# Performance work log

Measured on AMD Instinct MI355X. Metric: run time of the kernel, lower is better.

Reference implementation:

```python
import jax, jax.numpy as jnp
import numpy as np

B, M, D = 256, 256, 16
H1, H2 = 64, 64
HN = H1 // 2  # split_half keeps first half as next-layer state


def setup_inputs() -> dict:
    key = jax.random.key(0)
    ks = jax.random.split(key, 8)
    x = jax.random.normal(ks[0], (B, M), dtype=jnp.float32)
    emb = 0.02 * jax.random.normal(ks[1], (M, D), dtype=jnp.float32)  # field_embedding
    # Conv1d(kernel=1) weights squeezed to [out_ch, in_ch]
    def xavier(k, o, i):
        lim = np.sqrt(6.0 / (o + i)).astype(np.float32)
        return jax.random.uniform(k, (o, i), dtype=jnp.float32, minval=-lim, maxval=lim)
    W0 = xavier(ks[2], H1, M * M)      # layer 0: in_ch = m*m
    b0 = jnp.zeros((H1,), dtype=jnp.float32)
    W1 = xavier(ks[3], H2, HN * M)     # layer 1: in_ch = (H1//2)*m
    b1 = jnp.zeros((H2,), dtype=jnp.float32)
    out_width = (H1 - HN) + H2         # 32 + 64 = 96
    fcW = xavier(ks[4], 2, out_width)
    fcb = jnp.zeros((2,), dtype=jnp.float32)
    return {"x": x, "emb": emb, "W0": W0, "b0": b0, "W1": W1, "b1": b1, "fcW": fcW, "fcb": fcb}


def _cin_layer(Xk_prev, X0, W, b):
    # outer product over fields, flattened: Z [B, prev_H*m, d]
    Bd = X0.shape[0]
    Z = jnp.einsum('bhd,bmd->bhmd', Xk_prev, X0).reshape(Bd, -1, X0.shape[-1])
    # kernel-1 Conv1d == channel-mixing matmul per d slice, + bias, + relu
    return jax.nn.relu(jnp.einsum('bcd,oc->bod', Z, W) + b[None, :, None])


def reference(x, emb, W0, b0, W1, b1, fcW, fcb):
    X0 = jnp.einsum('bi,ij->bij', x, emb)          # [B, m, d]
    X1 = _cin_layer(X0, X0, W0, b0)                # [B, H1, d]
    out1 = X1[:, HN:, :]                            # direct output half
    Xp = X1[:, :HN, :]                              # hidden half feeds next layer
    X2 = _cin_layer(Xp, X0, W1, b1)                # [B, H2, d] (last layer: full output)
    cin_out = jnp.concatenate([out1.sum(axis=2), X2.sum(axis=2)], axis=1)  # [B, 96]
    return cin_out @ fcW.T + fcb
```

## Files before the change

### kernel.cpp

```cpp
#include <hip/hip_runtime.h>

typedef unsigned short u16;
typedef short bf16x8 __attribute__((ext_vector_type(8)));
typedef float f32x4 __attribute__((ext_vector_type(4)));

#define AS1 __attribute__((address_space(1)))
#define AS3 __attribute__((address_space(3)))

__device__ __forceinline__ u16 f2bf(float f) {
    unsigned u = __float_as_uint(f);
    u += 0x7fffu + ((u >> 16) & 1u);
    return (u16)(u >> 16);
}
__device__ __forceinline__ float bf2f(u16 h) {
    return __uint_as_float(((unsigned)h) << 16);
}

__device__ __forceinline__ void gload_lds16(const void* g, void* l) {
    __builtin_amdgcn_global_load_lds((AS1 unsigned int*)(g),
                                     (AS3 unsigned int*)(l), 16, 0, 0);
}

__global__ void cvt_bf16_kernel(const float* __restrict__ W0, const float* __restrict__ W1,
                                u16* __restrict__ W0b, u16* __restrict__ W1b) {
    int i = blockIdx.x * blockDim.x + threadIdx.x;
    const float* src; u16* dst; int j;
    if (i < 1048576) { src = W0; dst = W0b; j = i; }
    else             { src = W1; dst = W1b; j = i - 1048576; }
    float4 v = reinterpret_cast<const float4*>(src)[j];
    ushort4 o;
    o.x = f2bf(v.x); o.y = f2bf(v.y); o.z = f2bf(v.z); o.w = f2bf(v.w);
    reinterpret_cast<ushort4*>(dst)[j] = o;
}

__global__ void build_qt_kernel(const float* __restrict__ x, const float* __restrict__ emb,
                                u16* __restrict__ Qt, u16* __restrict__ E1) {
    int n = blockIdx.x;
    int b = n >> 4, d = n & 15;
    int m0 = threadIdx.x * 4;
    float4 xv = *reinterpret_cast<const float4*>(x + b * 256 + m0);
    ushort4 q;
    q.x = f2bf(xv.x * emb[(m0 + 0) * 16 + d]);
    q.y = f2bf(xv.y * emb[(m0 + 1) * 16 + d]);
    q.z = f2bf(xv.z * emb[(m0 + 2) * 16 + d]);
    q.w = f2bf(xv.w * emb[(m0 + 3) * 16 + d]);
    *reinterpret_cast<ushort4*>(Qt + n * 256 + m0) = q;
    int e1 = (n >> 8) * 65536 + (m0 >> 7) * 32768 + ((n >> 6) & 3) * 8192
           + ((m0 >> 4) & 7) * 1024 + ((n >> 4) & 3) * 256
           + ((((m0 >> 2) & 3) << 4) + (n & 15)) * 4;
    *reinterpret_cast<ushort4*>(E1 + e1) = q;
}

__global__ __launch_bounds__(512, 2) void cin1_kernel(
    const u16* __restrict__ W0b, const u16* __restrict__ Qt, const u16* __restrict__ E1,
    const float* __restrict__ b0, u16* __restrict__ E2, float* __restrict__ S1)
{
    __shared__ __attribute__((aligned(16))) u16 As[4][8192];
    __shared__ __attribute__((aligned(16))) u16 Bs[4][8192];
    __shared__ float part[2][256];

    const int tid = threadIdx.x, lane = tid & 63, w = tid >> 6;
    const int wh = w >> 2, wn = w & 3;
    const int lid = blockIdx.x;
    const int g8 = lid & 7, m = lid >> 3;
    const int o = ((g8 >> 1) << 4) | (m & 15);
    const int ntile = ((g8 & 1) << 3) | (m >> 4);

    const int dr = ((lane >> 3) << 1) | (lane & 1);
    const int dk = (((lane & 7) >> 1) ^ ((lane >> 3) & 3)) << 3;
    const u16* aSrc0 = W0b + (o * 256 + (w * 2 + 0) * 16 + dr) * 256 + dk;
    const u16* aSrc1 = W0b + (o * 256 + (w * 2 + 1) * 16 + dr) * 256 + dk;
    const u16* bSrc0 = Qt + (ntile * 256 + (w * 2 + 0) * 16 + dr) * 256 + dk;
    const u16* bSrc1 = Qt + (ntile * 256 + (w * 2 + 1) * 16 + dr) * 256 + dk;
    const int ldsA0 = (w * 2 + 0) * 512, ldsA1 = (w * 2 + 1) * 512;

    const int l2 = (lane & 15) >> 1;
    const int qu = (((((lane >> 4) ^ (l2 & 3)) << 1) | (lane & 1)) << 3);
    const int aOff = wh * 4096 + l2 * 64 + qu;
    const int bOff = wn * 2048 + l2 * 64 + qu;

    f32x4 zero = {0.f, 0.f, 0.f, 0.f};
    f32x4 acc[8][4];
#pragma unroll
    for (int f = 0; f < 8; ++f)
#pragma unroll
        for (int gg = 0; gg < 4; ++gg) acc[f][gg] = zero;

    auto stage = [&](int kc, int bb) {
        int ko = kc * 32;
        gload_lds16(aSrc0 + ko, &As[bb][ldsA0]);
        gload_lds16(aSrc1 + ko, &As[bb][ldsA1]);
        gload_lds16(bSrc0 + ko, &Bs[bb][ldsA0]);
        gload_lds16(bSrc1 + ko, &Bs[bb][ldsA1]);
    };

    stage(0, 0); stage(1, 1); stage(2, 2);
#pragma unroll
    for (int kc = 0; kc < 8; ++kc) {
        if (kc < 6)       asm volatile("s_waitcnt vmcnt(8)" ::: "memory");
        else if (kc == 6) asm volatile("s_waitcnt vmcnt(4)" ::: "memory");
        else              asm volatile("s_waitcnt vmcnt(0)" ::: "memory");
        __builtin_amdgcn_s_barrier();
        asm volatile("" ::: "memory");
        const u16* Ab = &As[kc & 3][0];
        const u16* Bb = &Bs[kc & 3][0];
        bf16x8 a[8], b[4];
#pragma unroll
        for (int f = 0; f < 8; ++f)
            a[f] = *reinterpret_cast<const bf16x8*>(Ab + aOff + f * 512);
#pragma unroll
        for (int gg = 0; gg < 4; ++gg)
            b[gg] = *reinterpret_cast<const bf16x8*>(Bb + bOff + gg * 512);
#pragma unroll
        for (int f = 0; f < 8; ++f)
#pragma unroll
            for (int gg = 0; gg < 4; ++gg)
                acc[f][gg] = __builtin_amdgcn_mfma_f32_16x16x32_bf16(a[f], b[gg], acc[f][gg], 0, 0, 0);
        if (kc < 5) stage(kc + 3, (kc + 3) & 3);
    }

    float psum[4] = {0.f, 0.f, 0.f, 0.f};
    const u16* eb = E1 + ntile * 65536 + wh * 32768 + wn * 8192 + lane * 4;
#pragma unroll
    for (int f = 0; f < 8; ++f)
#pragma unroll
        for (int gg = 0; gg < 4; ++gg) {
            ushort4 wv = *reinterpret_cast<const ushort4*>(eb + f * 1024 + gg * 256);
            psum[gg] += bf2f(wv.x) * acc[f][gg][0] + bf2f(wv.y) * acc[f][gg][1]
                      + bf2f(wv.z) * acc[f][gg][2] + bf2f(wv.w) * acc[f][gg][3];
        }
#pragma unroll
    for (int gg = 0; gg < 4; ++gg) {
        float p = psum[gg];
        p += __shfl_xor(p, 16);
        p += __shfl_xor(p, 32);
        if (lane < 16) part[wh][wn * 64 + gg * 16 + lane] = p;
    }
    __syncthreads();
    if (tid < 256) {
        const int nl = tid;
        float v = part[0][nl] + part[1][nl] + b0[o];
        float r = fmaxf(v, 0.0f);
        const int n = ntile * 256 + nl;
        if (o < 32) {
            int idx = ntile * 8192 + (o >> 4) * 4096 + (nl >> 6) * 1024 + ((nl >> 4) & 3) * 256
                    + ((((o >> 2) & 3) << 4) + (nl & 15)) * 4 + (o & 3);
            E2[idx] = f2bf(r);
        } else {
            float s = r;
            s += __shfl_xor(s, 1); s += __shfl_xor(s, 2);
            s += __shfl_xor(s, 4); s += __shfl_xor(s, 8);
            if ((nl & 15) == 0) S1[(n >> 4) * 32 + (o - 32)] = s;
        }
    }
}

__global__ __launch_bounds__(512, 2) void cin2_kernel(
    const u16* __restrict__ W1b, const u16* __restrict__ Qt, const u16* __restrict__ E2,
    const float* __restrict__ b1, float* __restrict__ S2)
{
    __shared__ __attribute__((aligned(16))) u16 As[4][4096];
    __shared__ __attribute__((aligned(16))) u16 Bs[4][8192];
    __shared__ float part[2][2][256];

    const int tid = threadIdx.x, lane = tid & 63, w = tid >> 6;
    const int wh = w >> 2, wn = w & 3;
    const int ntile = blockIdx.x & 15, og = blockIdx.x >> 4;

    const int dr = ((lane >> 3) << 1) | (lane & 1);
    const int dk = (((lane & 7) >> 1) ^ ((lane >> 3) & 3)) << 3;
    const u16* aSrc = W1b + (og * 128 + w * 16 + dr) * 256 + dk;
    const u16* bSrc0 = Qt + (ntile * 256 + (w * 2 + 0) * 16 + dr) * 256 + dk;
    const u16* bSrc1 = Qt + (ntile * 256 + (w * 2 + 1) * 16 + dr) * 256 + dk;
    const int ldsA = w * 512;
    const int ldsB0 = (w * 2 + 0) * 512, ldsB1 = (w * 2 + 1) * 512;

    const int l2 = (lane & 15) >> 1;
    const int qu = (((((lane >> 4) ^ (l2 & 3)) << 1) | (lane & 1)) << 3);
    const int aOff = wh * 2048 + l2 * 64 + qu;
    const int bOff = wn * 2048 + l2 * 64 + qu;

    f32x4 zero = {0.f, 0.f, 0.f, 0.f};
    f32x4 acc[4][4];
#pragma unroll
    for (int f = 0; f < 4; ++f)
#pragma unroll
        for (int gg = 0; gg < 4; ++gg) acc[f][gg] = zero;

    auto stage = [&](int kc, int bb) {
        int ko = kc * 32;
        gload_lds16(aSrc + ko, &As[bb][ldsA]);
        gload_lds16(bSrc0 + ko, &Bs[bb][ldsB0]);
        gload_lds16(bSrc1 + ko, &Bs[bb][ldsB1]);
    };

    stage(0, 0); stage(1, 1); stage(2, 2);
#pragma unroll
    for (int kc = 0; kc < 8; ++kc) {
        if (kc < 6)       asm volatile("s_waitcnt vmcnt(6)" ::: "memory");
        else if (kc == 6) asm volatile("s_waitcnt vmcnt(3)" ::: "memory");
        else              asm volatile("s_waitcnt vmcnt(0)" ::: "memory");
        __builtin_amdgcn_s_barrier();
        asm volatile("" ::: "memory");
        const u16* Ab = &As[kc & 3][0];
        const u16* Bb = &Bs[kc & 3][0];
        bf16x8 a[4], b[4];
#pragma unroll
        for (int f = 0; f < 4; ++f)
            a[f] = *reinterpret_cast<const bf16x8*>(Ab + aOff + f * 512);
#pragma unroll
        for (int gg = 0; gg < 4; ++gg)
            b[gg] = *reinterpret_cast<const bf16x8*>(Bb + bOff + gg * 512);
#pragma unroll
        for (int f = 0; f < 4; ++f)
#pragma unroll
            for (int gg = 0; gg < 4; ++gg)
                acc[f][gg] = __builtin_amdgcn_mfma_f32_16x16x32_bf16(a[f], b[gg], acc[f][gg], 0, 0, 0);
        if (kc < 5) stage(kc + 3, (kc + 3) & 3);
    }

    float psum[2][4] = {{0.f,0.f,0.f,0.f},{0.f,0.f,0.f,0.f}};
    const u16* eb = E2 + ntile * 8192 + wn * 1024 + lane * 4;
#pragma unroll
    for (int f = 0; f < 4; ++f)
#pragma unroll
        for (int gg = 0; gg < 4; ++gg) {
            ushort4 wv = *reinterpret_cast<const ushort4*>(eb + (f & 1) * 4096 + gg * 256);
            psum[f >> 1][gg] += bf2f(wv.x) * acc[f][gg][0] + bf2f(wv.y) * acc[f][gg][1]
                              + bf2f(wv.z) * acc[f][gg][2] + bf2f(wv.w) * acc[f][gg][3];
        }
#pragma unroll
    for (int ol = 0; ol < 2; ++ol)
#pragma unroll
        for (int gg = 0; gg < 4; ++gg) {
            float p = psum[ol][gg];
            p += __shfl_xor(p, 16);
            p += __shfl_xor(p, 32);
            if (lane < 16) part[wh][ol][wn * 64 + gg * 16 + lane] = p;
        }
    __syncthreads();
    if (tid < 256) {
        const int nl = tid;
        const int n = ntile * 256 + nl;
#pragma unroll
        for (int ol4 = 0; ol4 < 4; ++ol4) {
            const int oo = og * 4 + ol4;
            float v = part[ol4 >> 1][ol4 & 1][nl] + b1[oo];
            float r = fmaxf(v, 0.0f);
            float s = r;
            s += __shfl_xor(s, 1); s += __shfl_xor(s, 2);
            s += __shfl_xor(s, 4); s += __shfl_xor(s, 8);
            if ((nl & 15) == 0) S2[(n >> 4) * 64 + oo] = s;
        }
    }
}

__global__ void final_fc_kernel(const float* __restrict__ S1, const float* __restrict__ S2,
                                const float* __restrict__ fcW, const float* __restrict__ fcb,
                                float* __restrict__ out) {
    int b = threadIdx.x;
    float a0 = fcb[0], a1 = fcb[1];
#pragma unroll 8
    for (int c = 0; c < 32; ++c) {
        float v = S1[b * 32 + c];
        a0 += v * fcW[c]; a1 += v * fcW[96 + c];
    }
#pragma unroll 8
    for (int c = 0; c < 64; ++c) {
        float v = S2[b * 64 + c];
        a0 += v * fcW[32 + c]; a1 += v * fcW[96 + 32 + c];
    }
    out[b * 2 + 0] = a0;
    out[b * 2 + 1] = a1;
}

extern "C" void kernel_launch(void* const* d_in, const int* in_sizes, int n_in,
                              void* d_out, int out_size, void* d_ws, size_t ws_size,
                              hipStream_t stream) {
    const float* x   = (const float*)d_in[0];
    const float* emb = (const float*)d_in[1];
    const float* W0  = (const float*)d_in[2];
    const float* b0  = (const float*)d_in[3];
    const float* W1  = (const float*)d_in[4];
    const float* b1  = (const float*)d_in[5];
    const float* fcW = (const float*)d_in[6];
    const float* fcb = (const float*)d_in[7];
    float* out = (float*)d_out;

    char* ws = (char*)d_ws;
    u16*   W0b = (u16*)(ws);
    u16*   W1b = (u16*)(ws + 8388608);
    u16*   Qt  = (u16*)(ws + 9437184);
    u16*   E1  = (u16*)(ws + 11534336);
    u16*   E2  = (u16*)(ws + 13631488);
    float* S1  = (float*)(ws + 13893632);
    float* S2  = (float*)(ws + 13926400);

    cvt_bf16_kernel<<<4608, 256, 0, stream>>>(W0, W1, W0b, W1b);
    build_qt_kernel<<<4096, 64, 0, stream>>>(x, emb, Qt, E1);
    cin1_kernel<<<1024, 512, 0, stream>>>(W0b, Qt, E1, b0, E2, S1);
    cin2_kernel<<<256, 512, 0, stream>>>(W1b, Qt, E2, b1, S2);
    final_fc_kernel<<<1, 256, 0, stream>>>(S1, S2, fcW, fcb, out);
}
```

Baseline: 70.81 us.

## Merge prep kernels and double-buffer LDS fragment reads in CIN GEMMs

Measured after the change: 72.34 us. 1.02x slower.

```diff
diff --git a/kernel.cpp b/kernel.cpp
--- a/kernel.cpp
+++ b/kernel.cpp
@@ -21,34 +21,37 @@
                                      (AS3 unsigned int*)(l), 16, 0, 0);
 }
 
-__global__ void cvt_bf16_kernel(const float* __restrict__ W0, const float* __restrict__ W1,
-                                u16* __restrict__ W0b, u16* __restrict__ W1b) {
-    int i = blockIdx.x * blockDim.x + threadIdx.x;
-    const float* src; u16* dst; int j;
-    if (i < 1048576) { src = W0; dst = W0b; j = i; }
-    else             { src = W1; dst = W1b; j = i - 1048576; }
-    float4 v = reinterpret_cast<const float4*>(src)[j];
-    ushort4 o;
-    o.x = f2bf(v.x); o.y = f2bf(v.y); o.z = f2bf(v.z); o.w = f2bf(v.w);
-    reinterpret_cast<ushort4*>(dst)[j] = o;
-}
-
-__global__ void build_qt_kernel(const float* __restrict__ x, const float* __restrict__ emb,
-                                u16* __restrict__ Qt, u16* __restrict__ E1) {
-    int n = blockIdx.x;
-    int b = n >> 4, d = n & 15;
-    int m0 = threadIdx.x * 4;
-    float4 xv = *reinterpret_cast<const float4*>(x + b * 256 + m0);
-    ushort4 q;
-    q.x = f2bf(xv.x * emb[(m0 + 0) * 16 + d]);
-    q.y = f2bf(xv.y * emb[(m0 + 1) * 16 + d]);
-    q.z = f2bf(xv.z * emb[(m0 + 2) * 16 + d]);
-    q.w = f2bf(xv.w * emb[(m0 + 3) * 16 + d]);
-    *reinterpret_cast<ushort4*>(Qt + n * 256 + m0) = q;
-    int e1 = (n >> 8) * 65536 + (m0 >> 7) * 32768 + ((n >> 6) & 3) * 8192
-           + ((m0 >> 4) & 7) * 1024 + ((n >> 4) & 3) * 256
-           + ((((m0 >> 2) & 3) << 4) + (n & 15)) * 4;
-    *reinterpret_cast<ushort4*>(E1 + e1) = q;
+__global__ void prep_kernel(const float* __restrict__ W0, const float* __restrict__ W1,
+                            const float* __restrict__ x, const float* __restrict__ emb,
+                            u16* __restrict__ W0b, u16* __restrict__ W1b,
+                            u16* __restrict__ Qt, u16* __restrict__ E1) {
+    int gid = blockIdx.x;
+    if (gid < 4608) {
+        int i = gid * 256 + threadIdx.x;
+        const float* src; u16* dst; int j;
+        if (i < 1048576) { src = W0; dst = W0b; j = i; }
+        else             { src = W1; dst = W1b; j = i - 1048576; }
+        float4 v = reinterpret_cast<const float4*>(src)[j];
+        ushort4 o;
+        o.x = f2bf(v.x); o.y = f2bf(v.y); o.z = f2bf(v.z); o.w = f2bf(v.w);
+        reinterpret_cast<ushort4*>(dst)[j] = o;
+    } else {
+        int n = (gid - 4608) * 4 + (threadIdx.x >> 6);
+        int lane = threadIdx.x & 63;
+        int b = n >> 4, d = n & 15;
+        int m0 = lane * 4;
+        float4 xv = *reinterpret_cast<const float4*>(x + b * 256 + m0);
+        ushort4 q;
+        q.x = f2bf(xv.x * emb[(m0 + 0) * 16 + d]);
+        q.y = f2bf(xv.y * emb[(m0 + 1) * 16 + d]);
+        q.z = f2bf(xv.z * emb[(m0 + 2) * 16 + d]);
+        q.w = f2bf(xv.w * emb[(m0 + 3) * 16 + d]);
+        *reinterpret_cast<ushort4*>(Qt + n * 256 + m0) = q;
+        int e1 = (n >> 8) * 65536 + (m0 >> 7) * 32768 + ((n >> 6) & 3) * 8192
+               + ((m0 >> 4) & 7) * 1024 + ((n >> 4) & 3) * 256
+               + ((((m0 >> 2) & 3) << 4) + (n & 15)) * 4;
+        *reinterpret_cast<ushort4*>(E1 + e1) = q;
+    }
 }
 
 __global__ __launch_bounds__(512, 2) void cin1_kernel(
@@ -86,6 +89,8 @@
 #pragma unroll
         for (int gg = 0; gg < 4; ++gg) acc[f][gg] = zero;
 
+    bf16x8 a[2][8], b[2][4];
+
     auto stage = [&](int kc, int bb) {
         int ko = kc * 32;
         gload_lds16(aSrc0 + ko, &As[bb][ldsA0]);
@@ -94,30 +99,41 @@
         gload_lds16(bSrc1 + ko, &Bs[bb][ldsA1]);
     };
 
+#define PREREAD(kb, pb)                                                              \
+    {                                                                                \
+        const u16* Ab_ = &As[(kb) & 3][0];                                           \
+        const u16* Bb_ = &Bs[(kb) & 3][0];                                           \
+        _Pragma("unroll")                                                            \
+        for (int f_ = 0; f_ < 8; ++f_)                                               \
+            a[pb][f_] = *reinterpret_cast<const bf16x8*>(Ab_ + aOff + f_ * 512);     \
+        _Pragma("unroll")                                                            \
+        for (int g_ = 0; g_ < 4; ++g_)                                               \
+            b[pb][g_] = *reinterpret_cast<const bf16x8*>(Bb_ + bOff + g_ * 512);     \
+    }
+
     stage(0, 0); stage(1, 1); stage(2, 2);
+    asm volatile("s_waitcnt vmcnt(8)" ::: "memory");
+    __builtin_amdgcn_s_barrier();
+    asm volatile("" ::: "memory");
+    PREREAD(0, 0);
 #pragma unroll
     for (int kc = 0; kc < 8; ++kc) {
-        if (kc < 6)       asm volatile("s_waitcnt vmcnt(8)" ::: "memory");
-        else if (kc == 6) asm volatile("s_waitcnt vmcnt(4)" ::: "memory");
-        else              asm volatile("s_waitcnt vmcnt(0)" ::: "memory");
+        if (kc < 6) asm volatile("s_waitcnt vmcnt(4)" ::: "memory");
+        else        asm volatile("s_waitcnt vmcnt(0)" ::: "memory");
         __builtin_amdgcn_s_barrier();
         asm volatile("" ::: "memory");
-        const u16* Ab = &As[kc & 3][0];
-        const u16* Bb = &Bs[kc & 3][0];
-        bf16x8 a[8], b[4];
+        const int cur = kc & 1;
+        if (kc < 7) PREREAD(kc + 1, cur ^ 1);
+        __builtin_amdgcn_s_setprio(1);
 #pragma unroll
         for (int f = 0; f < 8; ++f)
-            a[f] = *reinterpret_cast<const bf16x8*>(Ab + aOff + f * 512);
-#pragma unroll
-        for (int gg = 0; gg < 4; ++gg)
-            b[gg] = *reinterpret_cast<const bf16x8*>(Bb + bOff + gg * 512);
-#pragma unroll
-        for (int f = 0; f < 8; ++f)
 #pragma unroll
             for (int gg = 0; gg < 4; ++gg)
-                acc[f][gg] = __builtin_amdgcn_mfma_f32_16x16x32_bf16(a[f], b[gg], acc[f][gg], 0, 0, 0);
+                acc[f][gg] = __builtin_amdgcn_mfma_f32_16x16x32_bf16(a[cur][f], b[cur][gg], acc[f][gg], 0, 0, 0);
+        __builtin_amdgcn_s_setprio(0);
         if (kc < 5) stage(kc + 3, (kc + 3) & 3);
     }
+#undef PREREAD
 
     float psum[4] = {0.f, 0.f, 0.f, 0.f};
     const u16* eb = E1 + ntile * 65536 + wh * 32768 + wn * 8192 + lane * 4;
@@ -187,6 +203,8 @@
 #pragma unroll
         for (int gg = 0; gg < 4; ++gg) acc[f][gg] = zero;
 
+    bf16x8 a[2][4], b[2][4];
+
     auto stage = [&](int kc, int bb) {
         int ko = kc * 32;
         gload_lds16(aSrc + ko, &As[bb][ldsA]);
@@ -194,30 +212,41 @@
         gload_lds16(bSrc1 + ko, &Bs[bb][ldsB1]);
     };
 
+#define PREREAD2(kb, pb)                                                             \
+    {                                                                                \
+        const u16* Ab_ = &As[(kb) & 3][0];                                           \
+        const u16* Bb_ = &Bs[(kb) & 3][0];                                           \
+        _Pragma("unroll")                                                            \
+        for (int f_ = 0; f_ < 4; ++f_)                                               \
+            a[pb][f_] = *reinterpret_cast<const bf16x8*>(Ab_ + aOff + f_ * 512);     \
+        _Pragma("unroll")                                                            \
+        for (int g_ = 0; g_ < 4; ++g_)                                               \
+            b[pb][g_] = *reinterpret_cast<const bf16x8*>(Bb_ + bOff + g_ * 512);     \
+    }
+
     stage(0, 0); stage(1, 1); stage(2, 2);
+    asm volatile("s_waitcnt vmcnt(6)" ::: "memory");
+    __builtin_amdgcn_s_barrier();
+    asm volatile("" ::: "memory");
+    PREREAD2(0, 0);
 #pragma unroll
     for (int kc = 0; kc < 8; ++kc) {
-        if (kc < 6)       asm volatile("s_waitcnt vmcnt(6)" ::: "memory");
-        else if (kc == 6) asm volatile("s_waitcnt vmcnt(3)" ::: "memory");
-        else              asm volatile("s_waitcnt vmcnt(0)" ::: "memory");
+        if (kc < 6) asm volatile("s_waitcnt vmcnt(3)" ::: "memory");
+        else        asm volatile("s_waitcnt vmcnt(0)" ::: "memory");
         __builtin_amdgcn_s_barrier();
         asm volatile("" ::: "memory");
-        const u16* Ab = &As[kc & 3][0];
-        const u16* Bb = &Bs[kc & 3][0];
-        bf16x8 a[4], b[4];
+        const int cur = kc & 1;
+        if (kc < 7) PREREAD2(kc + 1, cur ^ 1);
+        __builtin_amdgcn_s_setprio(1);
 #pragma unroll
         for (int f = 0; f < 4; ++f)
-            a[f] = *reinterpret_cast<const bf16x8*>(Ab + aOff + f * 512);
-#pragma unroll
-        for (int gg = 0; gg < 4; ++gg)
-            b[gg] = *reinterpret_cast<const bf16x8*>(Bb + bOff + gg * 512);
-#pragma unroll
-        for (int f = 0; f < 4; ++f)
 #pragma unroll
             for (int gg = 0; gg < 4; ++gg)
-                acc[f][gg] = __builtin_amdgcn_mfma_f32_16x16x32_bf16(a[f], b[gg], acc[f][gg], 0, 0, 0);
+                acc[f][gg] = __builtin_amdgcn_mfma_f32_16x16x32_bf16(a[cur][f], b[cur][gg], acc[f][gg], 0, 0, 0);
+        __builtin_amdgcn_s_setprio(0);
         if (kc < 5) stage(kc + 3, (kc + 3) & 3);
     }
+#undef PREREAD2
 
     float psum[2][4] = {{0.f,0.f,0.f,0.f},{0.f,0.f,0.f,0.f}};
     const u16* eb = E2 + ntile * 8192 + wn * 1024 + lane * 4;
@@ -296,8 +325,7 @@
     float* S1  = (float*)(ws + 13893632);
     float* S2  = (float*)(ws + 13926400);
 
-    cvt_bf16_kernel<<<4608, 256, 0, stream>>>(W0, W1, W0b, W1b);
-    build_qt_kernel<<<4096, 64, 0, stream>>>(x, emb, Qt, E1);
+    prep_kernel<<<5632, 256, 0, stream>>>(W0, W1, x, emb, W0b, W1b, Qt, E1);
     cin1_kernel<<<1024, 512, 0, stream>>>(W0b, Qt, E1, b0, E2, S1);
     cin2_kernel<<<256, 512, 0, stream>>>(W1b, Qt, E2, b1, S2);
     final_fc_kernel<<<1, 256, 0, stream>>>(S1, S2, fcW, fcb, out);
```

## Merge prep kernels and retile CIN GEMMs to smaller N tiles with triple buffering

Applied to the files above, without the earlier changes.

Measured after the change: 71.64 us. Within noise of the previous version (+1.2%).

```diff
diff --git a/kernel.cpp b/kernel.cpp
--- a/kernel.cpp
+++ b/kernel.cpp
@@ -21,108 +21,112 @@
                                      (AS3 unsigned int*)(l), 16, 0, 0);
 }
 
-__global__ void cvt_bf16_kernel(const float* __restrict__ W0, const float* __restrict__ W1,
-                                u16* __restrict__ W0b, u16* __restrict__ W1b) {
-    int i = blockIdx.x * blockDim.x + threadIdx.x;
-    const float* src; u16* dst; int j;
-    if (i < 1048576) { src = W0; dst = W0b; j = i; }
-    else             { src = W1; dst = W1b; j = i - 1048576; }
-    float4 v = reinterpret_cast<const float4*>(src)[j];
-    ushort4 o;
-    o.x = f2bf(v.x); o.y = f2bf(v.y); o.z = f2bf(v.z); o.w = f2bf(v.w);
-    reinterpret_cast<ushort4*>(dst)[j] = o;
-}
-
-__global__ void build_qt_kernel(const float* __restrict__ x, const float* __restrict__ emb,
-                                u16* __restrict__ Qt, u16* __restrict__ E1) {
-    int n = blockIdx.x;
-    int b = n >> 4, d = n & 15;
-    int m0 = threadIdx.x * 4;
-    float4 xv = *reinterpret_cast<const float4*>(x + b * 256 + m0);
-    ushort4 q;
-    q.x = f2bf(xv.x * emb[(m0 + 0) * 16 + d]);
-    q.y = f2bf(xv.y * emb[(m0 + 1) * 16 + d]);
-    q.z = f2bf(xv.z * emb[(m0 + 2) * 16 + d]);
-    q.w = f2bf(xv.w * emb[(m0 + 3) * 16 + d]);
-    *reinterpret_cast<ushort4*>(Qt + n * 256 + m0) = q;
-    int e1 = (n >> 8) * 65536 + (m0 >> 7) * 32768 + ((n >> 6) & 3) * 8192
-           + ((m0 >> 4) & 7) * 1024 + ((n >> 4) & 3) * 256
-           + ((((m0 >> 2) & 3) << 4) + (n & 15)) * 4;
-    *reinterpret_cast<ushort4*>(E1 + e1) = q;
-}
-
-__global__ __launch_bounds__(512, 2) void cin1_kernel(
+__global__ void prep_kernel(const float* __restrict__ W0, const float* __restrict__ W1,
+                            const float* __restrict__ x, const float* __restrict__ emb,
+                            u16* __restrict__ W0b, u16* __restrict__ W1b,
+                            u16* __restrict__ Qt, u16* __restrict__ E1) {
+    int gid = blockIdx.x;
+    if (gid < 4608) {
+        int i = gid * 256 + threadIdx.x;
+        const float* src; u16* dst; int j;
+        if (i < 1048576) { src = W0; dst = W0b; j = i; }
+        else             { src = W1; dst = W1b; j = i - 1048576; }
+        float4 v = reinterpret_cast<const float4*>(src)[j];
+        ushort4 o;
+        o.x = f2bf(v.x); o.y = f2bf(v.y); o.z = f2bf(v.z); o.w = f2bf(v.w);
+        reinterpret_cast<ushort4*>(dst)[j] = o;
+    } else {
+        int n = (gid - 4608) * 4 + (threadIdx.x >> 6);
+        int lane = threadIdx.x & 63;
+        int b = n >> 4, d = n & 15;
+        int m0 = lane * 4;
+        float4 xv = *reinterpret_cast<const float4*>(x + b * 256 + m0);
+        ushort4 q;
+        q.x = f2bf(xv.x * emb[(m0 + 0) * 16 + d]);
+        q.y = f2bf(xv.y * emb[(m0 + 1) * 16 + d]);
+        q.z = f2bf(xv.z * emb[(m0 + 2) * 16 + d]);
+        q.w = f2bf(xv.w * emb[(m0 + 3) * 16 + d]);
+        *reinterpret_cast<ushort4*>(Qt + n * 256 + m0) = q;
+        int e1 = (n >> 7) * 32768 + (m0 >> 6) * 8192 + ((n >> 6) & 1) * 4096
+               + ((m0 >> 4) & 3) * 1024 + ((n >> 4) & 3) * 256
+               + (((m0 >> 2) & 3) * 16 + (n & 15)) * 4;
+        *reinterpret_cast<ushort4*>(E1 + e1) = q;
+    }
+}
+
+__global__ __launch_bounds__(512, 4) void cin1_kernel(
     const u16* __restrict__ W0b, const u16* __restrict__ Qt, const u16* __restrict__ E1,
     const float* __restrict__ b0, u16* __restrict__ E2, float* __restrict__ S1)
 {
-    __shared__ __attribute__((aligned(16))) u16 As[4][8192];
-    __shared__ __attribute__((aligned(16))) u16 Bs[4][8192];
-    __shared__ float part[2][256];
+    __shared__ __attribute__((aligned(16))) u16 As[3][8192];
+    __shared__ __attribute__((aligned(16))) u16 Bs[3][4096];
+    __shared__ float part[4][128];
 
     const int tid = threadIdx.x, lane = tid & 63, w = tid >> 6;
-    const int wh = w >> 2, wn = w & 3;
-    const int lid = blockIdx.x;
-    const int g8 = lid & 7, m = lid >> 3;
-    const int o = ((g8 >> 1) << 4) | (m & 15);
-    const int ntile = ((g8 & 1) << 3) | (m >> 4);
-
-    const int dr = ((lane >> 3) << 1) | (lane & 1);
-    const int dk = (((lane & 7) >> 1) ^ ((lane >> 3) & 3)) << 3;
-    const u16* aSrc0 = W0b + (o * 256 + (w * 2 + 0) * 16 + dr) * 256 + dk;
-    const u16* aSrc1 = W0b + (o * 256 + (w * 2 + 1) * 16 + dr) * 256 + dk;
-    const u16* bSrc0 = Qt + (ntile * 256 + (w * 2 + 0) * 16 + dr) * 256 + dk;
-    const u16* bSrc1 = Qt + (ntile * 256 + (w * 2 + 1) * 16 + dr) * 256 + dk;
+    const int wh = w >> 1, wn = w & 1;
+    const int bid = blockIdx.x;
+    const int g8 = bid & 7, rest = bid >> 3;
+    const int o = g8 * 8 + (rest & 7);
+    const int ntile = rest >> 3;
+
+    const int rl = lane >> 2;
+    const int sw = ((lane & 3) ^ ((rl + (rl >> 2)) & 3)) << 3;
+    const u16* aS0 = W0b + (o * 256 + (w * 2 + 0) * 16 + rl) * 256 + sw;
+    const u16* aS1 = W0b + (o * 256 + (w * 2 + 1) * 16 + rl) * 256 + sw;
+    const u16* bS0 = Qt + (ntile * 128 + w * 16 + rl) * 256 + sw;
     const int ldsA0 = (w * 2 + 0) * 512, ldsA1 = (w * 2 + 1) * 512;
-
-    const int l2 = (lane & 15) >> 1;
-    const int qu = (((((lane >> 4) ^ (l2 & 3)) << 1) | (lane & 1)) << 3);
-    const int aOff = wh * 4096 + l2 * 64 + qu;
-    const int bOff = wn * 2048 + l2 * 64 + qu;
+    const int ldsB0 = w * 512;
+
+    const int rbA = wh * 64 + (lane & 15);
+    const int rbB = wn * 64 + (lane & 15);
+    const int sl = lane >> 4;
+    const int aOff = rbA * 32 + ((sl ^ ((rbA + (rbA >> 2)) & 3)) << 3);
+    const int bOff = rbB * 32 + ((sl ^ ((rbB + (rbB >> 2)) & 3)) << 3);
 
     f32x4 zero = {0.f, 0.f, 0.f, 0.f};
-    f32x4 acc[8][4];
-#pragma unroll
-    for (int f = 0; f < 8; ++f)
+    f32x4 acc[4][4];
+#pragma unroll
+    for (int f = 0; f < 4; ++f)
 #pragma unroll
         for (int gg = 0; gg < 4; ++gg) acc[f][gg] = zero;
 
     auto stage = [&](int kc, int bb) {
         int ko = kc * 32;
-        gload_lds16(aSrc0 + ko, &As[bb][ldsA0]);
-        gload_lds16(aSrc1 + ko, &As[bb][ldsA1]);
-        gload_lds16(bSrc0 + ko, &Bs[bb][ldsA0]);
-        gload_lds16(bSrc1 + ko, &Bs[bb][ldsA1]);
+        gload_lds16(aS0 + ko, &As[bb][ldsA0]);
+        gload_lds16(aS1 + ko, &As[bb][ldsA1]);
+        gload_lds16(bS0 + ko, &Bs[bb][ldsB0]);
     };
 
-    stage(0, 0); stage(1, 1); stage(2, 2);
+    stage(0, 0); stage(1, 1);
 #pragma unroll
     for (int kc = 0; kc < 8; ++kc) {
-        if (kc < 6)       asm volatile("s_waitcnt vmcnt(8)" ::: "memory");
-        else if (kc == 6) asm volatile("s_waitcnt vmcnt(4)" ::: "memory");
-        else              asm volatile("s_waitcnt vmcnt(0)" ::: "memory");
+        if (kc < 7) asm volatile("s_waitcnt vmcnt(3)" ::: "memory");
+        else        asm volatile("s_waitcnt vmcnt(0)" ::: "memory");
         __builtin_amdgcn_s_barrier();
         asm volatile("" ::: "memory");
-        const u16* Ab = &As[kc & 3][0];
-        const u16* Bb = &Bs[kc & 3][0];
-        bf16x8 a[8], b[4];
-#pragma unroll
-        for (int f = 0; f < 8; ++f)
+        if (kc < 6) stage(kc + 2, (kc + 2) % 3);
+        const u16* Ab = &As[kc % 3][0];
+        const u16* Bb = &Bs[kc % 3][0];
+        bf16x8 a[4], b[4];
+#pragma unroll
+        for (int f = 0; f < 4; ++f)
             a[f] = *reinterpret_cast<const bf16x8*>(Ab + aOff + f * 512);
 #pragma unroll
         for (int gg = 0; gg < 4; ++gg)
             b[gg] = *reinterpret_cast<const bf16x8*>(Bb + bOff + gg * 512);
-#pragma unroll
-        for (int f = 0; f < 8; ++f)
+        __builtin_amdgcn_s_setprio(1);
+#pragma unroll
+        for (int f = 0; f < 4; ++f)
 #pragma unroll
             for (int gg = 0; gg < 4; ++gg)
                 acc[f][gg] = __builtin_amdgcn_mfma_f32_16x16x32_bf16(a[f], b[gg], acc[f][gg], 0, 0, 0);
-        if (kc < 5) stage(kc + 3, (kc + 3) & 3);
+        __builtin_amdgcn_s_setprio(0);
     }
 
     float psum[4] = {0.f, 0.f, 0.f, 0.f};
-    const u16* eb = E1 + ntile * 65536 + wh * 32768 + wn * 8192 + lane * 4;
-#pragma unroll
-    for (int f = 0; f < 8; ++f)
+    const u16* eb = E1 + ntile * 32768 + wh * 8192 + wn * 4096 + lane * 4;
+#pragma unroll
+    for (int f = 0; f < 4; ++f)
 #pragma unroll
         for (int gg = 0; gg < 4; ++gg) {
             ushort4 wv = *reinterpret_cast<const ushort4*>(eb + f * 1024 + gg * 256);
@@ -137,15 +141,13 @@
         if (lane < 16) part[wh][wn * 64 + gg * 16 + lane] = p;
     }
     __syncthreads();
-    if (tid < 256) {
+    if (tid < 128) {
         const int nl = tid;
-        float v = part[0][nl] + part[1][nl] + b0[o];
+        float v = part[0][nl] + part[1][nl] + part[2][nl] + part[3][nl] + b0[o];
         float r = fmaxf(v, 0.0f);
-        const int n = ntile * 256 + nl;
+        const int n = ntile * 128 + nl;
         if (o < 32) {
-            int idx = ntile * 8192 + (o >> 4) * 4096 + (nl >> 6) * 1024 + ((nl >> 4) & 3) * 256
-                    + ((((o >> 2) & 3) << 4) + (nl & 15)) * 4 + (o & 3);
-            E2[idx] = f2bf(r);
+            E2[((ntile * 2 + (nl >> 6)) * 4 + ((nl >> 4) & 3)) * 512 + (nl & 15) * 32 + o] = f2bf(r);
         } else {
             float s = r;
             s += __shfl_xor(s, 1); s += __shfl_xor(s, 2);
@@ -155,30 +157,34 @@
     }
 }
 
-__global__ __launch_bounds__(512, 2) void cin2_kernel(
+__global__ __launch_bounds__(256, 4) void cin2_kernel(
     const u16* __restrict__ W1b, const u16* __restrict__ Qt, const u16* __restrict__ E2,
     const float* __restrict__ b1, float* __restrict__ S2)
 {
-    __shared__ __attribute__((aligned(16))) u16 As[4][4096];
-    __shared__ __attribute__((aligned(16))) u16 Bs[4][8192];
-    __shared__ float part[2][2][256];
+    __shared__ __attribute__((aligned(16))) u16 As[3][4096];
+    __shared__ __attribute__((aligned(16))) u16 Bs[3][4096];
+    __shared__ float part[2][2][128];
 
     const int tid = threadIdx.x, lane = tid & 63, w = tid >> 6;
-    const int wh = w >> 2, wn = w & 3;
-    const int ntile = blockIdx.x & 15, og = blockIdx.x >> 4;
-
-    const int dr = ((lane >> 3) << 1) | (lane & 1);
-    const int dk = (((lane & 7) >> 1) ^ ((lane >> 3) & 3)) << 3;
-    const u16* aSrc = W1b + (og * 128 + w * 16 + dr) * 256 + dk;
-    const u16* bSrc0 = Qt + (ntile * 256 + (w * 2 + 0) * 16 + dr) * 256 + dk;
-    const u16* bSrc1 = Qt + (ntile * 256 + (w * 2 + 1) * 16 + dr) * 256 + dk;
-    const int ldsA = w * 512;
-    const int ldsB0 = (w * 2 + 0) * 512, ldsB1 = (w * 2 + 1) * 512;
-
-    const int l2 = (lane & 15) >> 1;
-    const int qu = (((((lane >> 4) ^ (l2 & 3)) << 1) | (lane & 1)) << 3);
-    const int aOff = wh * 2048 + l2 * 64 + qu;
-    const int bOff = wn * 2048 + l2 * 64 + qu;
+    const int wh = w >> 1, wn = w & 1;
+    const int bid = blockIdx.x;
+    const int g8 = bid & 7, rest = bid >> 3;
+    const int og = g8 * 2 + (rest & 1);
+    const int ntile = rest >> 1;
+
+    const int rl = lane >> 2;
+    const int sw = ((lane & 3) ^ ((rl + (rl >> 2)) & 3)) << 3;
+    const u16* aS0 = W1b + (og * 128 + (w * 2 + 0) * 16 + rl) * 256 + sw;
+    const u16* aS1 = W1b + (og * 128 + (w * 2 + 1) * 16 + rl) * 256 + sw;
+    const u16* bS0 = Qt + (ntile * 128 + (w * 2 + 0) * 16 + rl) * 256 + sw;
+    const u16* bS1 = Qt + (ntile * 128 + (w * 2 + 1) * 16 + rl) * 256 + sw;
+    const int ldsI0 = (w * 2 + 0) * 512, ldsI1 = (w * 2 + 1) * 512;
+
+    const int rbA = wh * 64 + (lane & 15);
+    const int rbB = wn * 64 + (lane & 15);
+    const int sl = lane >> 4;
+    const int aOff = rbA * 32 + ((sl ^ ((rbA + (rbA >> 2)) & 3)) << 3);
+    const int bOff = rbB * 32 + ((sl ^ ((rbB + (rbB >> 2)) & 3)) << 3);
 
     f32x4 zero = {0.f, 0.f, 0.f, 0.f};
     f32x4 acc[4][4];
@@ -189,21 +195,22 @@
 
     auto stage = [&](int kc, int bb) {
         int ko = kc * 32;
-        gload_lds16(aSrc + ko, &As[bb][ldsA]);
-        gload_lds16(bSrc0 + ko, &Bs[bb][ldsB0]);
-        gload_lds16(bSrc1 + ko, &Bs[bb][ldsB1]);
+        gload_lds16(aS0 + ko, &As[bb][ldsI0]);
+        gload_lds16(aS1 + ko, &As[bb][ldsI1]);
+        gload_lds16(bS0 + ko, &Bs[bb][ldsI0]);
+        gload_lds16(bS1 + ko, &Bs[bb][ldsI1]);
     };
 
-    stage(0, 0); stage(1, 1); stage(2, 2);
+    stage(0, 0); stage(1, 1);
 #pragma unroll
     for (int kc = 0; kc < 8; ++kc) {
-        if (kc < 6)       asm volatile("s_waitcnt vmcnt(6)" ::: "memory");
-        else if (kc == 6) asm volatile("s_waitcnt vmcnt(3)" ::: "memory");
-        else              asm volatile("s_waitcnt vmcnt(0)" ::: "memory");
+        if (kc < 7) asm volatile("s_waitcnt vmcnt(4)" ::: "memory");
+        else        asm volatile("s_waitcnt vmcnt(0)" ::: "memory");
         __builtin_amdgcn_s_barrier();
         asm volatile("" ::: "memory");
-        const u16* Ab = &As[kc & 3][0];
-        const u16* Bb = &Bs[kc & 3][0];
+        if (kc < 6) stage(kc + 2, (kc + 2) % 3);
+        const u16* Ab = &As[kc % 3][0];
+        const u16* Bb = &Bs[kc % 3][0];
         bf16x8 a[4], b[4];
 #pragma unroll
         for (int f = 0; f < 4; ++f)
@@ -211,21 +218,22 @@
 #pragma unroll
         for (int gg = 0; gg < 4; ++gg)
             b[gg] = *reinterpret_cast<const bf16x8*>(Bb + bOff + gg * 512);
+        __builtin_amdgcn_s_setprio(1);
 #pragma unroll
         for (int f = 0; f < 4; ++f)
 #pragma unroll
             for (int gg = 0; gg < 4; ++gg)
                 acc[f][gg] = __builtin_amdgcn_mfma_f32_16x16x32_bf16(a[f], b[gg], acc[f][gg], 0, 0, 0);
-        if (kc < 5) stage(kc + 3, (kc + 3) & 3);
+        __builtin_amdgcn_s_setprio(0);
     }
 
     float psum[2][4] = {{0.f,0.f,0.f,0.f},{0.f,0.f,0.f,0.f}};
-    const u16* eb = E2 + ntile * 8192 + wn * 1024 + lane * 4;
+    const u16* eb = E2 + (ntile * 2 + wn) * 2048 + (lane & 15) * 32 + (lane >> 4) * 4;
 #pragma unroll
     for (int f = 0; f < 4; ++f)
 #pragma unroll
         for (int gg = 0; gg < 4; ++gg) {
-            ushort4 wv = *reinterpret_cast<const ushort4*>(eb + (f & 1) * 4096 + gg * 256);
+            ushort4 wv = *reinterpret_cast<const ushort4*>(eb + gg * 512 + (f & 1) * 16);
             psum[f >> 1][gg] += bf2f(wv.x) * acc[f][gg][0] + bf2f(wv.y) * acc[f][gg][1]
                               + bf2f(wv.z) * acc[f][gg][2] + bf2f(wv.w) * acc[f][gg][3];
         }
@@ -239,13 +247,13 @@
             if (lane < 16) part[wh][ol][wn * 64 + gg * 16 + lane] = p;
         }
     __syncthreads();
-    if (tid < 256) {
+    if (tid < 128) {
         const int nl = tid;
-        const int n = ntile * 256 + nl;
-#pragma unroll
-        for (int ol4 = 0; ol4 < 4; ++ol4) {
-            const int oo = og * 4 + ol4;
-            float v = part[ol4 >> 1][ol4 & 1][nl] + b1[oo];
+        const int n = ntile * 128 + nl;
+#pragma unroll
+        for (int o4 = 0; o4 < 4; ++o4) {
+            const int oo = og * 4 + o4;
+            float v = part[o4 >> 1][o4 & 1][nl] + b1[oo];
             float r = fmaxf(v, 0.0f);
             float s = r;
             s += __shfl_xor(s, 1); s += __shfl_xor(s, 2);
@@ -296,9 +304,8 @@
     float* S1  = (float*)(ws + 13893632);
     float* S2  = (float*)(ws + 13926400);
 
-    cvt_bf16_kernel<<<4608, 256, 0, stream>>>(W0, W1, W0b, W1b);
-    build_qt_kernel<<<4096, 64, 0, stream>>>(x, emb, Qt, E1);
-    cin1_kernel<<<1024, 512, 0, stream>>>(W0b, Qt, E1, b0, E2, S1);
-    cin2_kernel<<<256, 512, 0, stream>>>(W1b, Qt, E2, b1, S2);
+    prep_kernel<<<5632, 256, 0, stream>>>(W0, W1, x, emb, W0b, W1b, Qt, E1);
+    cin1_kernel<<<2048, 512, 0, stream>>>(W0b, Qt, E1, b0, E2, S1);
+    cin2_kernel<<<512, 256, 0, stream>>>(W1b, Qt, E2, b1, S2);
     final_fc_kernel<<<1, 256, 0, stream>>>(S1, S2, fcW, fcb, out);
 }
```
